# Kernel tuning notes

Hardware: AMD Instinct MI355X
Metric: run time of the kernel (lower is better)

Reference implementation:

```python
import jax, jax.numpy as jnp
import numpy as np

B, E, H, N = 16, 1024, 16, 2048
Eh = E // H   # head dim = 64
BH = B * H    # 256


def setup_inputs() -> dict:
    key = jax.random.key(0)
    ks = jax.random.split(key, 12)
    query = jax.random.normal(ks[0], (B, E), jnp.float32)
    key_in = jax.random.normal(ks[1], (B, E), jnp.float32)
    value = jax.random.normal(ks[2], (B, E), jnp.float32)
    # State as it would look in steady state: a_sum ~ O(N) positive,
    # q_mem stores already-scaled queries (small), k/v unit-ish scale.
    a_sum_mem = float(N) * (0.9 + 0.2 * jax.random.uniform(ks[3], (BH, N - 1), jnp.float32))
    av_mem = (0.1 * float(N)) * jax.random.normal(ks[4], (BH, N - 1, Eh), jnp.float32)
    q_mem = 0.06 * jax.random.normal(ks[5], (BH, N, Eh), jnp.float32)
    k_t_mem = 0.5 * jax.random.normal(ks[6], (BH, Eh, N), jnp.float32)
    v_mem = 0.5 * jax.random.normal(ks[7], (BH, N, Eh), jnp.float32)
    in_proj_weight = 0.02 * jax.random.normal(ks[8], (3 * E, E), jnp.float32)
    in_proj_bias = jnp.zeros((3 * E,), jnp.float32)
    out_proj_weight = 0.02 * jax.random.normal(ks[9], (E, E), jnp.float32)
    out_proj_bias = jnp.zeros((E,), jnp.float32)
    return dict(query=query, key=key_in, value=value,
                a_sum_mem=a_sum_mem, av_mem=av_mem, q_mem=q_mem,
                k_t_mem=k_t_mem, v_mem=v_mem,
                in_proj_weight=in_proj_weight, in_proj_bias=in_proj_bias,
                out_proj_weight=out_proj_weight, out_proj_bias=out_proj_bias)


def _sdpa_step(a_sum_mem, av_mem, q_mem, k_t_mem, v_mem, q_step, k_step, v_step):
    # Faithful port of _scaled_dot_product_attention_step.
    q_step = q_step / jnp.sqrt(jnp.float32(Eh))          # (BH, Eh)
    q_old = q_mem[:, 0]                                   # (BH, Eh)
    k_old = k_t_mem[:, :, 0]                              # (BH, Eh)
    q_sel = jnp.stack((q_old, q_step), axis=1)            # (BH, 2, Eh)
    k_sel = jnp.stack((k_old, k_step), axis=2)            # (BH, Eh, 2)
    a_tb = jnp.exp(jnp.einsum('bte,bes->bts', q_sel, k_t_mem[:, :, 1:]))  # (BH, 2, N-1)
    a_lr = jnp.exp(jnp.einsum('bne,bet->bnt', q_mem[:, 1:, :], k_sel))    # (BH, N-1, 2)
    a_br = jnp.exp(jnp.sum(q_step * k_step, axis=1))      # (BH,)
    a_sum = jnp.concatenate(
        [a_sum_mem + a_lr[:, :, 1] - a_lr[:, :, 0],
         (a_tb[:, 1].sum(axis=1) + a_br)[:, None]], axis=1)               # (BH, N)
    av_top = (av_mem
              - a_lr[:, :, 0, None] * v_mem[:, 0][:, None, :]
              + a_lr[:, :, 1, None] * v_step[:, None, :])                 # (BH, N-1, Eh)
    av_bot = jnp.einsum('bs,bse->be', a_tb[:, 1], v_mem[:, 1:]) + a_br[:, None] * v_step
    av = jnp.concatenate([av_top, av_bot[:, None, :]], axis=1)            # (BH, N, Eh)
    out = av / a_sum[..., None]
    new_state = (a_sum[:, 1:], av[:, 1:],
                 jnp.concatenate([q_mem[:, 1:], q_step[:, None, :]], axis=1),
                 jnp.concatenate([k_t_mem[:, :, 1:], k_step[:, :, None]], axis=2),
                 jnp.concatenate([v_mem[:, 1:], v_step[:, None, :]], axis=1))
    return out, new_state


def reference(query, key, value, a_sum_mem, av_mem, q_mem, k_t_mem, v_mem,
              in_proj_weight, in_proj_bias, out_proj_weight, out_proj_bias):
    # Packed in-projection (q/k/v chunks of the packed weight).
    w_q, w_k, w_v = jnp.split(in_proj_weight, 3, axis=0)
    b_q, b_k, b_v = jnp.split(in_proj_bias, 3)
    q = (query @ w_q.T + b_q).reshape(BH, Eh)   # head split: (B, H*Eh) -> (B*H, Eh)
    k = (key @ w_k.T + b_k).reshape(BH, Eh)
    v = (value @ w_v.T + b_v).reshape(BH, Eh)
    attn, new_state = _sdpa_step(a_sum_mem, av_mem, q_mem, k_t_mem, v_mem, q, k, v)
    # (BH, N, Eh) -> (N, BH, Eh) -> (N, B, E), then output projection.
    attn = attn.transpose(1, 0, 2).reshape(N, B, E)
    out = attn @ out_proj_weight.T + out_proj_bias    # (N, B, E)
    return (out,) + new_state
```

## Files before the change

kernel.cpp:

```cpp
#include <hip/hip_runtime.h>
#include <hip/hip_bf16.h>

constexpr int kB  = 16;
constexpr int kE  = 1024;
constexpr int kH  = 16;
constexpr int kN  = 2048;
constexpr int kEh = 64;
constexpr int kBH = 256;
constexpr int kM  = kN * kB;

typedef __bf16 bf16x8 __attribute__((ext_vector_type(8)));
typedef float  f32x4  __attribute__((ext_vector_type(4)));

__global__ __launch_bounds__(256) void proj_kernel(
    const float* __restrict__ query, const float* __restrict__ key_in,
    const float* __restrict__ value, const float* __restrict__ W,
    const float* __restrict__ bias,
    float* __restrict__ q_step, float* __restrict__ k_step,
    float* __restrict__ v_step) {
  int j   = blockIdx.x;
  int mat = j >> 10;
  int col = j & 1023;
  const float* in = (mat == 0) ? query : ((mat == 1) ? key_in : value);
  const float* wrow = W + (size_t)j * kE;

  float part[16];
#pragma unroll
  for (int r = 0; r < 16; ++r) part[r] = 0.f;

  for (int k = threadIdx.x; k < kE; k += 256) {
    float w = wrow[k];
#pragma unroll
    for (int r = 0; r < 16; ++r) part[r] += w * in[r * kE + k];
  }
#pragma unroll
  for (int r = 0; r < 16; ++r) {
    float v = part[r];
    for (int off = 32; off > 0; off >>= 1) v += __shfl_down(v, off, 64);
    part[r] = v;
  }
  __shared__ float red[4][16];
  int wave = threadIdx.x >> 6;
  int lane = threadIdx.x & 63;
  if (lane == 0) {
#pragma unroll
    for (int r = 0; r < 16; ++r) red[wave][r] = part[r];
  }
  __syncthreads();
  if (threadIdx.x < 16) {
    int r = threadIdx.x;
    float v = red[0][r] + red[1][r] + red[2][r] + red[3][r] + bias[j];
    int h = col >> 6, eh = col & 63;
    int bh = r * kH + h;
    if (mat == 0)      q_step[bh * kEh + eh] = v * 0.125f;
    else if (mat == 1) k_step[bh * kEh + eh] = v;
    else               v_step[bh * kEh + eh] = v;
  }
}

__global__ void wcvt_kernel(const float* __restrict__ w,
                            __hip_bfloat16* __restrict__ o, int n) {
  int i = blockIdx.x * blockDim.x + threadIdx.x;
  if (i < n) o[i] = __float2bfloat16(w[i]);
}

__global__ __launch_bounds__(256) void kt_kernel(
    const float* __restrict__ k_t_mem, const float* __restrict__ q_step,
    float* __restrict__ k_t_out, float* __restrict__ a_tb1,
    float* __restrict__ top_sum) {
  int b = blockIdx.x;
  int chunk = blockIdx.y;
  __shared__ float qs[64];
  if (threadIdx.x < 64) qs[threadIdx.x] = q_step[b * kEh + threadIdx.x];
  __syncthreads();

  int c0 = chunk * 512;
  int c_a = c0 + threadIdx.x;
  int c_b = c0 + 256 + threadIdx.x;
  const float* src = k_t_mem + (size_t)b * kEh * kN;
  float* dst = k_t_out + (size_t)b * kEh * kN;

  float dot0 = 0.f, dot1 = 0.f;
  for (int e = 0; e < 64; ++e) {
    float va = src[(size_t)e * kN + c_a];
    float vb = src[(size_t)e * kN + c_b];
    dot0 += qs[e] * va;
    dot1 += qs[e] * vb;
    if (c_a >= 1) dst[(size_t)e * kN + c_a - 1] = va;
    dst[(size_t)e * kN + c_b - 1] = vb;
  }
  float t0 = (c_a >= 1) ? __expf(dot0) : 0.f;
  float t1 = __expf(dot1);
  if (c_a >= 1) a_tb1[(size_t)b * (kN - 1) + c_a - 1] = t0;
  a_tb1[(size_t)b * (kN - 1) + c_b - 1] = t1;

  float s = t0 + t1;
  for (int off = 32; off > 0; off >>= 1) s += __shfl_xor(s, off, 64);
  __shared__ float red[4];
  int wave = threadIdx.x >> 6, lane = threadIdx.x & 63;
  if (lane == 0) red[wave] = s;
  __syncthreads();
  if (threadIdx.x == 0)
    atomicAdd(&top_sum[b], red[0] + red[1] + red[2] + red[3]);
}

__global__ __launch_bounds__(256) void qav_kernel(
    const float* __restrict__ q_mem, const float* __restrict__ av_mem,
    const float* __restrict__ a_sum_mem, const float* __restrict__ k_t_mem,
    const float* __restrict__ v_mem, const float* __restrict__ k_step,
    const float* __restrict__ v_step, float* __restrict__ q_out,
    float* __restrict__ av_out, float* __restrict__ a_sum_out,
    __hip_bfloat16* __restrict__ attn) {
  int b = blockIdx.x;
  int chunk = blockIdx.y;
  int wave = threadIdx.x >> 6, lane = threadIdx.x & 63;
  int b_ = b >> 4, h = b & 15;

  float kold = k_t_mem[(size_t)b * kEh * kN + (size_t)lane * kN];
  float kst  = k_step[b * kEh + lane];
  float vold = v_mem[(size_t)b * kN * kEh + lane];
  float vst  = v_step[b * kEh + lane];

  int j0 = chunk * 32 + wave * 8;
  for (int jj = 0; jj < 8; ++jj) {
    int j = j0 + jj;
    if (j > kN - 2) break;
    float qv = q_mem[((size_t)b * kN + (j + 1)) * kEh + lane];
    float p0 = qv * kold;
    float p1 = qv * kst;
    for (int off = 32; off > 0; off >>= 1) {
      p0 += __shfl_xor(p0, off, 64);
      p1 += __shfl_xor(p1, off, 64);
    }
    float a0 = __expf(p0);
    float a1 = __expf(p1);
    q_out[((size_t)b * kN + j) * kEh + lane] = qv;
    float asum = a_sum_mem[(size_t)b * (kN - 1) + j] + a1 - a0;
    float avv = av_mem[((size_t)b * (kN - 1) + j) * kEh + lane]
                - a0 * vold + a1 * vst;
    attn[((size_t)j * kB + b_) * kE + h * kEh + lane] =
        __float2bfloat16(avv / asum);
    if (j >= 1) {
      if (lane == 0) a_sum_out[(size_t)b * (kN - 1) + (j - 1)] = asum;
      av_out[((size_t)b * (kN - 1) + (j - 1)) * kEh + lane] = avv;
    }
  }
}

__global__ __launch_bounds__(256) void v_kernel(
    const float* __restrict__ v_mem, const float* __restrict__ a_tb1,
    float* __restrict__ v_out, float* __restrict__ av_last) {
  int b = blockIdx.x;
  int chunk = blockIdx.y;
  int wave = threadIdx.x >> 6, lane = threadIdx.x & 63;
  const float* vsrc = v_mem + (size_t)b * kN * kEh;
  float* vdst = v_out + (size_t)b * kN * kEh;
  const float* tb = a_tb1 + (size_t)b * (kN - 1);

  float acc = 0.f;
  int s0 = chunk * 256 + wave * 64;
  for (int ss = 0; ss < 64; ++ss) {
    int s = s0 + ss;
    if (s > kN - 2) break;
    float t = tb[s];
    float vv = vsrc[(size_t)(s + 1) * kEh + lane];
    acc += t * vv;
    vdst[(size_t)s * kEh + lane] = vv;
  }
  __shared__ float red[4][64];
  red[wave][lane] = acc;
  __syncthreads();
  if (wave == 0) {
    float a = red[0][lane] + red[1][lane] + red[2][lane] + red[3][lane];
    atomicAdd(&av_last[b * kEh + lane], a);
  }
}

__global__ __launch_bounds__(64) void final_kernel(
    const float* __restrict__ q_step, const float* __restrict__ k_step,
    const float* __restrict__ v_step, const float* __restrict__ top_sum,
    const float* __restrict__ av_last_in, float* __restrict__ q_out,
    float* __restrict__ k_t_out, float* __restrict__ v_out,
    float* __restrict__ a_sum_out, float* __restrict__ av_out,
    __hip_bfloat16* __restrict__ attn) {
  int b = blockIdx.x;
  int lane = threadIdx.x;
  int b_ = b >> 4, h = b & 15;
  float qs = q_step[b * kEh + lane];
  float ks = k_step[b * kEh + lane];
  float vs = v_step[b * kEh + lane];
  float p = qs * ks;
  for (int off = 32; off > 0; off >>= 1) p += __shfl_xor(p, off, 64);
  float abr = __expf(p);
  float asum = top_sum[b] + abr;
  float avl = av_last_in[b * kEh + lane] + abr * vs;
  attn[((size_t)(kN - 1) * kB + b_) * kE + h * kEh + lane] =
      __float2bfloat16(avl / asum);
  if (lane == 0) a_sum_out[(size_t)b * (kN - 1) + (kN - 2)] = asum;
  av_out[((size_t)b * (kN - 1) + (kN - 2)) * kEh + lane] = avl;
  q_out[((size_t)b * kN + (kN - 1)) * kEh + lane] = qs;
  k_t_out[(size_t)b * kEh * kN + (size_t)lane * kN + (kN - 1)] = ks;
  v_out[((size_t)b * kN + (kN - 1)) * kEh + lane] = vs;
}

#define BM 128
#define BN 128
#define BK 64

__global__ __launch_bounds__(256) void gemm_kernel(
    const __bf16* __restrict__ A, const __bf16* __restrict__ Bw,
    const float* __restrict__ bias, float* __restrict__ C,
    int M, int Ncols, int K) {
  __shared__ __bf16 lA[BM * BK];
  __shared__ __bf16 lB[BN * BK];
  int tid = threadIdx.x;
  int m0 = blockIdx.x * BM;
  int n0 = blockIdx.y * BN;
  int wave = tid >> 6;
  int lane = tid & 63;
  int wm = (wave & 1) * 64;
  int wn = (wave >> 1) * 64;

  f32x4 zero = {0.f, 0.f, 0.f, 0.f};
  f32x4 acc[4][4];
#pragma unroll
  for (int i = 0; i < 4; ++i)
#pragma unroll
    for (int j = 0; j < 4; ++j) acc[i][j] = zero;

  int quad = lane >> 4;
  int mrow = lane & 15;

  for (int k0 = 0; k0 < K; k0 += BK) {
#pragma unroll
    for (int r = 0; r < 4; ++r) {
      int off = r * 4096 + tid * 16;
      int row = off >> 7;
      int col8 = (off >> 4) & 7;
      const __bf16* ga = A + ((size_t)(m0 + row) * K + k0 + col8 * 8);
      const __bf16* gb = Bw + ((size_t)(n0 + row) * K + k0 + col8 * 8);
      __builtin_amdgcn_global_load_lds(
          (const __attribute__((address_space(1))) void*)ga,
          (__attribute__((address_space(3))) void*)((char*)lA + off), 16, 0, 0);
      __builtin_amdgcn_global_load_lds(
          (const __attribute__((address_space(1))) void*)gb,
          (__attribute__((address_space(3))) void*)((char*)lB + off), 16, 0, 0);
    }
    __syncthreads();

#pragma unroll
    for (int kk = 0; kk < 2; ++kk) {
      bf16x8 af[4], bfr[4];
#pragma unroll
      for (int i = 0; i < 4; ++i) {
        af[i]  = *(const bf16x8*)(&lA[(wm + i * 16 + mrow) * BK + kk * 32 + quad * 8]);
        bfr[i] = *(const bf16x8*)(&lB[(wn + i * 16 + mrow) * BK + kk * 32 + quad * 8]);
      }
#pragma unroll
      for (int i = 0; i < 4; ++i)
#pragma unroll
        for (int j = 0; j < 4; ++j)
          acc[i][j] = __builtin_amdgcn_mfma_f32_16x16x32_bf16(
              af[i], bfr[j], acc[i][j], 0, 0, 0);
    }
    __syncthreads();
  }

  int colq = lane & 15;
  int rowq = lane >> 4;
#pragma unroll
  for (int i = 0; i < 4; ++i) {
#pragma unroll
    for (int j = 0; j < 4; ++j) {
      int col = n0 + wn + j * 16 + colq;
      float bv = bias[col];
      size_t base = (size_t)(m0 + wm + i * 16 + rowq * 4) * Ncols + col;
#pragma unroll
      for (int r = 0; r < 4; ++r) {
        C[base + (size_t)r * Ncols] = acc[i][j][r] + bv;
      }
    }
  }
}

extern "C" void kernel_launch(void* const* d_in, const int* in_sizes, int n_in,
                              void* d_out, int out_size, void* d_ws,
                              size_t ws_size, hipStream_t stream) {
  const float* query          = (const float*)d_in[0];
  const float* key_in         = (const float*)d_in[1];
  const float* value          = (const float*)d_in[2];
  const float* a_sum_mem      = (const float*)d_in[3];
  const float* av_mem         = (const float*)d_in[4];
  const float* q_mem          = (const float*)d_in[5];
  const float* k_t_mem        = (const float*)d_in[6];
  const float* v_mem          = (const float*)d_in[7];
  const float* in_proj_weight = (const float*)d_in[8];
  const float* in_proj_bias   = (const float*)d_in[9];
  const float* out_proj_weight= (const float*)d_in[10];
  const float* out_proj_bias  = (const float*)d_in[11];

  float* out       = (float*)d_out;
  float* a_sum_out = out + (size_t)kN * kB * kE;
  float* av_out    = a_sum_out + (size_t)kBH * (kN - 1);
  float* q_out     = av_out + (size_t)kBH * (kN - 1) * kEh;
  float* k_t_out   = q_out + (size_t)kBH * kN * kEh;
  float* v_out     = k_t_out + (size_t)kBH * kEh * kN;

  char* ws = (char*)d_ws;
  float* q_step  = (float*)ws;
  float* k_step  = q_step + 16384;
  float* v_step  = k_step + 16384;
  float* top_sum = v_step + 16384;
  float* av_last = top_sum + 256;
  float* a_tb1   = av_last + 16384;
  __hip_bfloat16* wo_bf   = (__hip_bfloat16*)(ws + 2359296);
  __hip_bfloat16* attn_bf = (__hip_bfloat16*)(ws + 4456448);

  hipMemsetAsync(ws + 196608, 0, 66560, stream);

  proj_kernel<<<3 * kE, 256, 0, stream>>>(query, key_in, value, in_proj_weight,
                                          in_proj_bias, q_step, k_step, v_step);
  wcvt_kernel<<<(kE * kE) / 256, 256, 0, stream>>>(out_proj_weight, wo_bf,
                                                   kE * kE);
  kt_kernel<<<dim3(kBH, 4), 256, 0, stream>>>(k_t_mem, q_step, k_t_out, a_tb1,
                                              top_sum);
  qav_kernel<<<dim3(kBH, 64), 256, 0, stream>>>(q_mem, av_mem, a_sum_mem,
                                                k_t_mem, v_mem, k_step, v_step,
                                                q_out, av_out, a_sum_out,
                                                attn_bf);
  v_kernel<<<dim3(kBH, 8), 256, 0, stream>>>(v_mem, a_tb1, v_out, av_last);
  final_kernel<<<kBH, 64, 0, stream>>>(q_step, k_step, v_step, top_sum,
                                       av_last, q_out, k_t_out, v_out,
                                       a_sum_out, av_out, attn_bf);
  gemm_kernel<<<dim3(kM / BM, kE / BN), 256, 0, stream>>>(
      (const __bf16*)attn_bf, (const __bf16*)wo_bf, out_proj_bias, out, kM, kE,
      kE);
}
```

Measured before the change: 1.202 ms.

## Vectorize memory-bound state-update kernels with float4 loads and stores

Rewrites the projection, k_t shift, q/av update and v shift kernels to use 128-bit float4 loads and stores, with sub-wave groups of 16 lanes each handling one row. The k_t shift builds each shifted vector from an aligned float4 plus one neighbour element. The qav and kt grids are halved so each thread covers more columns. This aims to cut memory instruction count and improve bandwidth on the large state copies, at the cost of extra shuffles, edge-case predicates and some redundant loads.

```diff
diff --git a/kernel.cpp b/kernel.cpp
--- a/kernel.cpp
+++ b/kernel.cpp
@@ -11,6 +11,12 @@
 
 typedef __bf16 bf16x8 __attribute__((ext_vector_type(8)));
 typedef float  f32x4  __attribute__((ext_vector_type(4)));
+
+static __device__ __forceinline__ unsigned short bf16_bits(float f) {
+  union { __hip_bfloat16 h; unsigned short u; } cv;
+  cv.h = __float2bfloat16(f);
+  return cv.u;
+}
 
 __global__ __launch_bounds__(256) void proj_kernel(
     const float* __restrict__ query, const float* __restrict__ key_in,
@@ -23,15 +29,14 @@
   int col = j & 1023;
   const float* in = (mat == 0) ? query : ((mat == 1) ? key_in : value);
   const float* wrow = W + (size_t)j * kE;
-
+  int tid = threadIdx.x;
+
+  float4 w4 = reinterpret_cast<const float4*>(wrow)[tid];
   float part[16];
 #pragma unroll
-  for (int r = 0; r < 16; ++r) part[r] = 0.f;
-
-  for (int k = threadIdx.x; k < kE; k += 256) {
-    float w = wrow[k];
-#pragma unroll
-    for (int r = 0; r < 16; ++r) part[r] += w * in[r * kE + k];
+  for (int r = 0; r < 16; ++r) {
+    float4 in4 = reinterpret_cast<const float4*>(in + (size_t)r * kE)[tid];
+    part[r] = w4.x * in4.x + w4.y * in4.y + w4.z * in4.z + w4.w * in4.w;
   }
 #pragma unroll
   for (int r = 0; r < 16; ++r) {
@@ -74,27 +79,36 @@
   if (threadIdx.x < 64) qs[threadIdx.x] = q_step[b * kEh + threadIdx.x];
   __syncthreads();
 
-  int c0 = chunk * 512;
-  int c_a = c0 + threadIdx.x;
-  int c_b = c0 + 256 + threadIdx.x;
+  int c4 = (chunk * 256 + threadIdx.x) * 4;
+  bool last = (c4 + 4 >= kN);
   const float* src = k_t_mem + (size_t)b * kEh * kN;
   float* dst = k_t_out + (size_t)b * kEh * kN;
 
-  float dot0 = 0.f, dot1 = 0.f;
+  f32x4 dot = {0.f, 0.f, 0.f, 0.f};
+#pragma unroll 4
   for (int e = 0; e < 64; ++e) {
-    float va = src[(size_t)e * kN + c_a];
-    float vb = src[(size_t)e * kN + c_b];
-    dot0 += qs[e] * va;
-    dot1 += qs[e] * vb;
-    if (c_a >= 1) dst[(size_t)e * kN + c_a - 1] = va;
-    dst[(size_t)e * kN + c_b - 1] = vb;
-  }
-  float t0 = (c_a >= 1) ? __expf(dot0) : 0.f;
-  float t1 = __expf(dot1);
-  if (c_a >= 1) a_tb1[(size_t)b * (kN - 1) + c_a - 1] = t0;
-  a_tb1[(size_t)b * (kN - 1) + c_b - 1] = t1;
-
-  float s = t0 + t1;
+    float4 a = reinterpret_cast<const float4*>(src + (size_t)e * kN)[c4 >> 2];
+    float s3 = last ? 0.f : src[(size_t)e * kN + c4 + 4];
+    float4 sh = {a.y, a.z, a.w, s3};
+    reinterpret_cast<float4*>(dst + (size_t)e * kN)[c4 >> 2] = sh;
+    float q = qs[e];
+    dot.x += q * sh.x;
+    dot.y += q * sh.y;
+    dot.z += q * sh.z;
+    dot.w += q * sh.w;
+  }
+  float tx = __expf(dot.x);
+  float ty = __expf(dot.y);
+  float tz = __expf(dot.z);
+  float tw = last ? 0.f : __expf(dot.w);
+
+  float* tbrow = a_tb1 + (size_t)b * (kN - 1);
+  tbrow[c4 + 0] = tx;
+  tbrow[c4 + 1] = ty;
+  tbrow[c4 + 2] = tz;
+  if (!last) tbrow[c4 + 3] = tw;
+
+  float s = tx + ty + tz + tw;
   for (int off = 32; off > 0; off >>= 1) s += __shfl_xor(s, off, 64);
   __shared__ float red[4];
   int wave = threadIdx.x >> 6, lane = threadIdx.x & 63;
@@ -114,35 +128,63 @@
   int b = blockIdx.x;
   int chunk = blockIdx.y;
   int wave = threadIdx.x >> 6, lane = threadIdx.x & 63;
+  int g = lane >> 4, c = lane & 15;
   int b_ = b >> 4, h = b & 15;
 
-  float kold = k_t_mem[(size_t)b * kEh * kN + (size_t)lane * kN];
-  float kst  = k_step[b * kEh + lane];
-  float vold = v_mem[(size_t)b * kN * kEh + lane];
-  float vst  = v_step[b * kEh + lane];
-
-  int j0 = chunk * 32 + wave * 8;
-  for (int jj = 0; jj < 8; ++jj) {
-    int j = j0 + jj;
-    if (j > kN - 2) break;
-    float qv = q_mem[((size_t)b * kN + (j + 1)) * kEh + lane];
-    float p0 = qv * kold;
-    float p1 = qv * kst;
-    for (int off = 32; off > 0; off >>= 1) {
+  float4 kst  = reinterpret_cast<const float4*>(k_step + (size_t)b * kEh)[c];
+  float4 vst  = reinterpret_cast<const float4*>(v_step + (size_t)b * kEh)[c];
+  float4 vold = reinterpret_cast<const float4*>(v_mem + (size_t)b * kN * kEh)[c];
+  const float* kt0 = k_t_mem + (size_t)b * kEh * kN;
+  float4 kold;
+  kold.x = kt0[(size_t)(4 * c + 0) * kN];
+  kold.y = kt0[(size_t)(4 * c + 1) * kN];
+  kold.z = kt0[(size_t)(4 * c + 2) * kN];
+  kold.w = kt0[(size_t)(4 * c + 3) * kN];
+
+  unsigned short* attn_u = reinterpret_cast<unsigned short*>(attn);
+
+  int jb = chunk * 64 + wave * 16;
+#pragma unroll
+  for (int it = 0; it < 4; ++it) {
+    int j = jb + it * 4 + g;
+    bool valid = (j <= kN - 2);
+    int jc = valid ? j : (kN - 2);
+
+    float4 q4 = reinterpret_cast<const float4*>(
+        q_mem + ((size_t)b * kN + (jc + 1)) * kEh)[c];
+    float p0 = q4.x * kold.x + q4.y * kold.y + q4.z * kold.z + q4.w * kold.w;
+    float p1 = q4.x * kst.x + q4.y * kst.y + q4.z * kst.z + q4.w * kst.w;
+#pragma unroll
+    for (int off = 1; off < 16; off <<= 1) {
       p0 += __shfl_xor(p0, off, 64);
       p1 += __shfl_xor(p1, off, 64);
     }
     float a0 = __expf(p0);
     float a1 = __expf(p1);
-    q_out[((size_t)b * kN + j) * kEh + lane] = qv;
-    float asum = a_sum_mem[(size_t)b * (kN - 1) + j] + a1 - a0;
-    float avv = av_mem[((size_t)b * (kN - 1) + j) * kEh + lane]
-                - a0 * vold + a1 * vst;
-    attn[((size_t)j * kB + b_) * kE + h * kEh + lane] =
-        __float2bfloat16(avv / asum);
-    if (j >= 1) {
-      if (lane == 0) a_sum_out[(size_t)b * (kN - 1) + (j - 1)] = asum;
-      av_out[((size_t)b * (kN - 1) + (j - 1)) * kEh + lane] = avv;
+    float asum = a_sum_mem[(size_t)b * (kN - 1) + jc] + a1 - a0;
+    float4 av4 = reinterpret_cast<const float4*>(
+        av_mem + ((size_t)b * (kN - 1) + jc) * kEh)[c];
+    float4 avv;
+    avv.x = av4.x - a0 * vold.x + a1 * vst.x;
+    avv.y = av4.y - a0 * vold.y + a1 * vst.y;
+    avv.z = av4.z - a0 * vold.z + a1 * vst.z;
+    avv.w = av4.w - a0 * vold.w + a1 * vst.w;
+
+    if (valid) {
+      reinterpret_cast<float4*>(q_out + ((size_t)b * kN + jc) * kEh)[c] = q4;
+      float inv = 1.0f / asum;
+      ushort4 pk;
+      pk.x = bf16_bits(avv.x * inv);
+      pk.y = bf16_bits(avv.y * inv);
+      pk.z = bf16_bits(avv.z * inv);
+      pk.w = bf16_bits(avv.w * inv);
+      *reinterpret_cast<ushort4*>(
+          attn_u + ((size_t)jc * kB + b_) * kE + h * kEh + c * 4) = pk;
+      if (j >= 1) {
+        reinterpret_cast<float4*>(
+            av_out + ((size_t)b * (kN - 1) + (jc - 1)) * kEh)[c] = avv;
+        if (c == 0) a_sum_out[(size_t)b * (kN - 1) + (jc - 1)] = asum;
+      }
     }
   }
 }
@@ -153,26 +195,45 @@
   int b = blockIdx.x;
   int chunk = blockIdx.y;
   int wave = threadIdx.x >> 6, lane = threadIdx.x & 63;
+  int g = lane >> 4, c = lane & 15;
   const float* vsrc = v_mem + (size_t)b * kN * kEh;
   float* vdst = v_out + (size_t)b * kN * kEh;
   const float* tb = a_tb1 + (size_t)b * (kN - 1);
 
-  float acc = 0.f;
-  int s0 = chunk * 256 + wave * 64;
-  for (int ss = 0; ss < 64; ++ss) {
-    int s = s0 + ss;
-    if (s > kN - 2) break;
-    float t = tb[s];
-    float vv = vsrc[(size_t)(s + 1) * kEh + lane];
-    acc += t * vv;
-    vdst[(size_t)s * kEh + lane] = vv;
-  }
-  __shared__ float red[4][64];
-  red[wave][lane] = acc;
+  f32x4 acc = {0.f, 0.f, 0.f, 0.f};
+  int sbase = chunk * 256 + wave * 64;
+#pragma unroll 4
+  for (int it = 0; it < 16; ++it) {
+    int s = sbase + it * 4 + g;
+    bool valid = (s <= kN - 2);
+    int sc = valid ? s : (kN - 2);
+    float t = valid ? tb[sc] : 0.f;
+    float4 vv = reinterpret_cast<const float4*>(vsrc + (size_t)(sc + 1) * kEh)[c];
+    acc.x += t * vv.x;
+    acc.y += t * vv.y;
+    acc.z += t * vv.z;
+    acc.w += t * vv.w;
+    if (valid)
+      reinterpret_cast<float4*>(vdst + (size_t)sc * kEh)[c] = vv;
+  }
+#pragma unroll
+  for (int off = 16; off <= 32; off <<= 1) {
+    acc.x += __shfl_xor(acc.x, off, 64);
+    acc.y += __shfl_xor(acc.y, off, 64);
+    acc.z += __shfl_xor(acc.z, off, 64);
+    acc.w += __shfl_xor(acc.w, off, 64);
+  }
+  __shared__ f32x4 red[4][16];
+  if (g == 0) red[wave][c] = acc;
   __syncthreads();
-  if (wave == 0) {
-    float a = red[0][lane] + red[1][lane] + red[2][lane] + red[3][lane];
-    atomicAdd(&av_last[b * kEh + lane], a);
+  if (threadIdx.x < 16) {
+    f32x4 a0 = red[0][threadIdx.x], a1 = red[1][threadIdx.x];
+    f32x4 a2 = red[2][threadIdx.x], a3 = red[3][threadIdx.x];
+    float* dst = av_last + (size_t)b * kEh + threadIdx.x * 4;
+    atomicAdd(dst + 0, a0.x + a1.x + a2.x + a3.x);
+    atomicAdd(dst + 1, a0.y + a1.y + a2.y + a3.y);
+    atomicAdd(dst + 2, a0.z + a1.z + a2.z + a3.z);
+    atomicAdd(dst + 3, a0.w + a1.w + a2.w + a3.w);
   }
 }
 
@@ -322,9 +383,9 @@
                                           in_proj_bias, q_step, k_step, v_step);
   wcvt_kernel<<<(kE * kE) / 256, 256, 0, stream>>>(out_proj_weight, wo_bf,
                                                    kE * kE);
-  kt_kernel<<<dim3(kBH, 4), 256, 0, stream>>>(k_t_mem, q_step, k_t_out, a_tb1,
+  kt_kernel<<<dim3(kBH, 2), 256, 0, stream>>>(k_t_mem, q_step, k_t_out, a_tb1,
                                               top_sum);
-  qav_kernel<<<dim3(kBH, 64), 256, 0, stream>>>(q_mem, av_mem, a_sum_mem,
+  qav_kernel<<<dim3(kBH, 32), 256, 0, stream>>>(q_mem, av_mem, a_sum_mem,
                                                 k_t_mem, v_mem, k_step, v_step,
                                                 q_out, av_out, a_sum_out,
                                                 attn_bf);
```

After: 1.172 ms. 1.03x faster.
